# Performance work log

Measured on AMD Instinct MI355X. Metric: run time of the kernel, lower is better.

The kernel has to match this reference:

```python
import jax, jax.numpy as jnp
import numpy as np

N_NODES = 50000


def _relgraphconv(x, W, Wloop, b, src, dst, etypes, n_nodes):
    # DGL RelGraphConv (regularizer=None, self_loop=True, norm=None):
    # out[i] = sum over incoming edges (j->i, rel r) of W_r @ x[j]  +  W_loop @ x[i]  +  b
    # low-mem form: transform all nodes per relation, then gather per edge.
    h_rel = jnp.einsum('ni,rio->rno', x, W)          # [R, N, out]
    msg = h_rel[etypes, src]                          # [E, out]
    agg = jax.ops.segment_sum(msg, dst, num_segments=n_nodes)  # [N, out]
    return agg + x @ Wloop + b


def setup_inputs() -> dict:
    key = jax.random.key(0)
    ks = jax.random.split(key, 12)
    N, E, n_state = N_NODES, 800000, 128
    inp = {
        'x': jax.random.normal(ks[0], (N, n_state), dtype=jnp.float32),
        'src': jax.random.randint(ks[1], (E,), 0, N, dtype=jnp.int32),
        'dst': jax.random.randint(ks[2], (E,), 0, N, dtype=jnp.int32),
        'etypes': jax.random.randint(ks[3], (E,), 0, 2, dtype=jnp.int32),
        'cell_size': jax.random.randint(ks[4], (N,), 0, 8, dtype=jnp.int32),
        'max_size': jax.random.randint(ks[5], (N,), 0, 8, dtype=jnp.int32),
        'W1': jax.random.normal(ks[6], (2, n_state, 64), dtype=jnp.float32) * 0.05,
        'loop1': jax.random.normal(ks[7], (n_state, 64), dtype=jnp.float32) * 0.05,
        'b1': jnp.zeros((64,), dtype=jnp.float32),
        'W2': jax.random.normal(ks[8], (2, 64, 64), dtype=jnp.float32) * 0.05,
        'loop2': jax.random.normal(ks[9], (64, 64), dtype=jnp.float32) * 0.05,
        'b2': jnp.zeros((64,), dtype=jnp.float32),
        'W3': jax.random.normal(ks[10], (2, 64, 2), dtype=jnp.float32) * 0.05,
        'loop3': jax.random.normal(ks[11], (64, 2), dtype=jnp.float32) * 0.05,
        'b3': jnp.zeros((2,), dtype=jnp.float32),
    }
    return inp


def reference(x, src, dst, etypes, cell_size, max_size,
              W1, loop1, b1, W2, loop2, b2, W3, loop3, b3):
    N = x.shape[0]
    h = jax.nn.relu(_relgraphconv(x, W1, loop1, b1, src, dst, etypes, N))
    h = jax.nn.relu(_relgraphconv(h, W2, loop2, b2, src, dst, etypes, N))
    h = _relgraphconv(h, W3, loop3, b3, src, dst, etypes, N)   # [N, 2]
    # action mask: col 0 = cannot upsize, col 1 = cannot downsize
    upper = cell_size >= (max_size - 1)
    lower = cell_size == 0
    mask = jnp.stack([upper, lower], axis=1)                   # [N, 2] bool
    return jnp.where(mask, h.min() - 1.0, h)
```

## Files before the change

### kernel.cpp

```cpp
#include <hip/hip_runtime.h>


#define STRIDE 64
#define BINCAP 2560

typedef unsigned short ushortT;
typedef __attribute__((ext_vector_type(8))) short short8;
typedef __attribute__((ext_vector_type(4))) float f32x4;

__device__ inline ushortT f2bf(float f) {
    union { float f; unsigned u; } v; v.f = f;
    unsigned r = v.u + 0x7FFFu + ((v.u >> 16) & 1u);
    return (ushortT)(r >> 16);
}
__device__ inline float bf2f(ushortT h) {
    union { unsigned u; float f; } v; v.u = ((unsigned)h) << 16;
    return v.f;
}

__device__ inline void atomicMinF(float* addr, float v) {
    if (v >= 0.f) atomicMin((int*)addr, __float_as_int(v));
    else          atomicMax((unsigned int*)addr, __float_as_uint(v));
}

__global__ __launch_bounds__(256) void pack_init_kernel(
    const float* __restrict__ W1, const float* __restrict__ loop1,
    const float* __restrict__ W2, const float* __restrict__ loop2,
    ushortT* __restrict__ BP1, ushortT* __restrict__ BP2,
    int* __restrict__ bincnt, float* __restrict__ minval,
    int* __restrict__ done, int NBINS) {
    int g = (int)blockIdx.x * 256 + (int)threadIdx.x;
    if (g < NBINS) bincnt[g] = 0;
    if (g == 0) { *(int*)minval = 0x7f7f7f7f; *done = 0; }
    if (g < 3072) {
        int l = g & 63, ks = (g >> 6) & 3, ct = g >> 8;
        int c = ct * 16 + (l & 15);
        int mat = c >> 6, cc = c & 63;
        int kbase = ks * 32 + (l >> 4) * 8;
        ushortT* dstp = BP1 + (size_t)g * 8;
#pragma unroll
        for (int j = 0; j < 8; ++j) {
            int k = kbase + j;
            float v = (mat < 2) ? W1[((size_t)mat * 128 + k) * 64 + cc]
                                : loop1[(size_t)k * 64 + cc];
            dstp[j] = f2bf(v);
        }
    } else {
        int s = g - 3072;
        int l = s & 63, ks = (s >> 6) & 1, ct = s >> 7;
        int c = ct * 16 + (l & 15);
        int mat = c >> 6, cc = c & 63;
        int kbase = ks * 32 + (l >> 4) * 8;
        ushortT* dstp = BP2 + (size_t)s * 8;
#pragma unroll
        for (int j = 0; j < 8; ++j) {
            int k = kbase + j;
            float v = (mat < 2) ? W2[((size_t)mat * 64 + k) * 64 + cc]
                                : loop2[(size_t)k * 64 + cc];
            dstp[j] = f2bf(v);
        }
    }
}

__global__ __launch_bounds__(256) void k1_kernel(
    const float* __restrict__ x, const ushortT* __restrict__ BP1,
    const float* __restrict__ b1,
    ushortT* __restrict__ hrelb, ushortT* __restrict__ H1b,
    const int* __restrict__ src, const int* __restrict__ dst,
    const int* __restrict__ et, int* __restrict__ bincnt, int2* __restrict__ binbuf,
    int N, int E, int NBINS, int NBA) {
    __shared__ int hist[512];
    __shared__ int gbase[512];
    __shared__ ushortT rnk[4096];

    const int t = (int)threadIdx.x;

    if ((int)blockIdx.x < NBA) {
        for (int i = t; i < NBINS; i += 256) hist[i] = 0;
        __syncthreads();
        const int base = (int)blockIdx.x * 4096;
#pragma unroll
        for (int i = 0; i < 16; ++i) {
            int e = base + t + i * 256;
            if (e < E) {
                int bb = dst[e] >> 7;
                rnk[t + i * 256] = (ushortT)atomicAdd(&hist[bb], 1);
            }
        }
        __syncthreads();
        for (int i = t; i < NBINS; i += 256) {
            int h = hist[i];
            gbase[i] = h ? atomicAdd(&bincnt[i], h) : 0;
        }
        __syncthreads();
#pragma unroll
        for (int i = 0; i < 16; ++i) {
            int e = base + t + i * 256;
            if (e < E) {
                int dd = dst[e];
                int bb = dd >> 7;
                int v = et[e] * N + src[e];
                int pos = gbase[bb] + (int)rnk[t + i * 256];
                if (pos < BINCAP)
                    binbuf[(size_t)bb * BINCAP + pos] = make_int2(dd, v);
            }
        }
        return;
    }
    const int w = t >> 6, lane = t & 63;
    const int rowbase = (((int)blockIdx.x - NBA) * 4 + w) * 16;
    const int m = lane & 15, quad = lane >> 4;
    const int nclamp = min(rowbase + m, N - 1);

    short8 a[4];
    const float* xp = x + (size_t)nclamp * 128 + quad * 8;
#pragma unroll
    for (int ks = 0; ks < 4; ++ks) {
        float4 g0 = *(const float4*)(xp + ks * 32);
        float4 g1 = *(const float4*)(xp + ks * 32 + 4);
        a[ks][0] = (short)f2bf(g0.x); a[ks][1] = (short)f2bf(g0.y);
        a[ks][2] = (short)f2bf(g0.z); a[ks][3] = (short)f2bf(g0.w);
        a[ks][4] = (short)f2bf(g1.x); a[ks][5] = (short)f2bf(g1.y);
        a[ks][6] = (short)f2bf(g1.z); a[ks][7] = (short)f2bf(g1.w);
    }

    f32x4 acc[12];
#pragma unroll
    for (int ct = 0; ct < 12; ++ct) acc[ct] = (f32x4){0.f, 0.f, 0.f, 0.f};

#pragma unroll
    for (int ks = 0; ks < 4; ++ks) {
#pragma unroll
        for (int ct = 0; ct < 12; ++ct) {
            short8 b = *(const short8*)&BP1[((size_t)(ct * 4 + ks) * 64 + lane) * 8];
            acc[ct] = __builtin_amdgcn_mfma_f32_16x16x32_bf16(a[ks], b, acc[ct], 0, 0, 0);
        }
    }

    const int node0 = rowbase + quad * 4;
#pragma unroll
    for (int ct = 0; ct < 12; ++ct) {
        int c = ct * 16 + m;
        int mat = c >> 6, cc = c & 63;
        float bias = (mat == 2) ? b1[cc] : 0.f;
#pragma unroll
        for (int j = 0; j < 4; ++j) {
            int n = node0 + j;
            if (n < N) {
                float v = acc[ct][j] + bias;
                if (mat < 2) hrelb[((size_t)mat * N + n) * 64 + cc] = f2bf(v);
                else         H1b[(size_t)n * 64 + cc] = f2bf(v);
            }
        }
    }
}

__global__ __launch_bounds__(512, 4) void ag2_kernel(
    const ushortT* __restrict__ hrelb, const ushortT* __restrict__ H1b,
    const ushortT* __restrict__ BP2, const float* __restrict__ b2,
    const int* __restrict__ bincnt, const int2* __restrict__ binbuf,
    int* __restrict__ eidx, int* __restrict__ cnt,
    ushortT* __restrict__ hrel2b, ushortT* __restrict__ H2b, int N) {
    __shared__ int lcnt[64];
    __shared__ int lidx[64][STRIDE];
    __shared__ __align__(16) ushortT Hs[64][72];

    const int t = (int)threadIdx.x;
    const int B = (int)blockIdx.x;
    const int nodeBase = B * 64;
    const int bin = B >> 1;

    if (t < 64) lcnt[t] = 0;
    __syncthreads();

    const int cb = min(bincnt[bin], BINCAP);
    const int2* buf = binbuf + (size_t)bin * BINCAP;
    for (int i = t; i < cb; i += 512) {
        int2 rec = buf[i];
        int local = rec.x - nodeBase;
        if ((unsigned)local < 64u) {
            int r = atomicAdd(&lcnt[local], 1);
            if (r < STRIDE) {
                lidx[local][r] = rec.y;
                eidx[(size_t)rec.x * STRIDE + r] = rec.y;
            }
        }
    }
    __syncthreads();
    if (t < 64) {
        int c = min(lcnt[t], STRIDE);
        lcnt[t] = c;
        int node = nodeBase + t;
        if (node < N) cnt[node] = c;
    }
    __syncthreads();

    const int w = t >> 6, lane = t & 63;

    for (int i = 0; i < 8; ++i) {
        int local = w * 8 + i;
        int node = nodeBase + local;
        if (node >= N) { Hs[local][lane] = 0; continue; }
        int deg = lcnt[local];
        float acc = bf2f(H1b[(size_t)node * 64 + lane]);
        int j = 0;
        for (; j + 7 < deg; j += 8) {
            float v[8];
#pragma unroll
            for (int q = 0; q < 8; ++q) {
                int id = lidx[local][j + q];
                v[q] = bf2f(hrelb[(size_t)id * 64 + lane]);
            }
            acc += ((v[0] + v[1]) + (v[2] + v[3])) + ((v[4] + v[5]) + (v[6] + v[7]));
        }
        for (; j < deg; ++j)
            acc += bf2f(hrelb[(size_t)lidx[local][j] * 64 + lane]);
        Hs[local][lane] = f2bf(fmaxf(acc, 0.f));
    }
    __syncthreads();

    const int rt = w & 3, h = w >> 2;
    const int m = lane & 15, quad = lane >> 4;
    short8 a[2];
#pragma unroll
    for (int ks = 0; ks < 2; ++ks)
        a[ks] = *(const short8*)&Hs[rt * 16 + m][quad * 8 + ks * 32];

    f32x4 acc[6];
#pragma unroll
    for (int c6 = 0; c6 < 6; ++c6) acc[c6] = (f32x4){0.f, 0.f, 0.f, 0.f};

#pragma unroll
    for (int ks = 0; ks < 2; ++ks) {
#pragma unroll
        for (int c6 = 0; c6 < 6; ++c6) {
            int ct = h * 6 + c6;
            short8 b = *(const short8*)&BP2[((size_t)(ct * 2 + ks) * 64 + lane) * 8];
            acc[c6] = __builtin_amdgcn_mfma_f32_16x16x32_bf16(a[ks], b, acc[c6], 0, 0, 0);
        }
    }

    const int node0 = nodeBase + rt * 16 + quad * 4;
#pragma unroll
    for (int c6 = 0; c6 < 6; ++c6) {
        int ct = h * 6 + c6;
        int c = ct * 16 + m;
        int mat = c >> 6, cc = c & 63;
        float bias = (mat == 2) ? b2[cc] : 0.f;
#pragma unroll
        for (int j = 0; j < 4; ++j) {
            int n = node0 + j;
            if (n < N) {
                float v = acc[c6][j] + bias;
                if (mat < 2) hrel2b[((size_t)mat * N + n) * 64 + cc] = f2bf(v);
                else         H2b[(size_t)n * 64 + cc] = f2bf(v);
            }
        }
    }
}

__global__ void k3_kernel(const ushortT* __restrict__ hrel2b, const ushortT* __restrict__ H2b,
                          const int* __restrict__ eidx, const int* __restrict__ cnt,
                          const float* __restrict__ W3, const float* __restrict__ loop3,
                          const float* __restrict__ b3,
                          float* __restrict__ hrel3, float* __restrict__ H3, int N) {
    int node = (int)blockIdx.x * 4 + ((int)threadIdx.x >> 6);
    if (node >= N) return;
    int lane = (int)threadIdx.x & 63;
    int deg = cnt[node];
    int my = (lane < deg) ? eidx[(size_t)node * STRIDE + lane] : 0;
    float acc = bf2f(H2b[(size_t)node * 64 + lane]);
    int j = 0;
    for (; j + 7 < deg; j += 8) {
        int id[8];
        float v[8];
#pragma unroll
        for (int q = 0; q < 8; ++q) id[q] = __shfl(my, j + q, 64);
#pragma unroll
        for (int q = 0; q < 8; ++q) v[q] = bf2f(hrel2b[(size_t)id[q] * 64 + lane]);
        acc += ((v[0] + v[1]) + (v[2] + v[3])) + ((v[4] + v[5]) + (v[6] + v[7]));
    }
    for (; j < deg; ++j)
        acc += bf2f(hrel2b[(size_t)__shfl(my, j, 64) * 64 + lane]);
    float xk = fmaxf(acc, 0.f);
    float p[6];
    p[0] = xk * W3[lane * 2 + 0];
    p[1] = xk * W3[lane * 2 + 1];
    p[2] = xk * W3[(64 + lane) * 2 + 0];
    p[3] = xk * W3[(64 + lane) * 2 + 1];
    p[4] = xk * loop3[lane * 2 + 0];
    p[5] = xk * loop3[lane * 2 + 1];
#pragma unroll
    for (int mm = 32; mm >= 1; mm >>= 1) {
#pragma unroll
        for (int q = 0; q < 6; ++q) p[q] += __shfl_xor(p[q], mm, 64);
    }
    if (lane == 0) {
        hrel3[(size_t)node * 2 + 0] = p[0];
        hrel3[(size_t)node * 2 + 1] = p[1];
        hrel3[((size_t)N + node) * 2 + 0] = p[2];
        hrel3[((size_t)N + node) * 2 + 1] = p[3];
        H3[(size_t)node * 2 + 0] = p[4] + b3[0];
        H3[(size_t)node * 2 + 1] = p[5] + b3[1];
    }
}

__global__ __launch_bounds__(256) void a3m_mask_kernel(
    const float* __restrict__ hrel3, const int* __restrict__ eidx,
    const int* __restrict__ cnt, const float* __restrict__ H3,
    const int* __restrict__ cs, const int* __restrict__ ms,
    float* __restrict__ minval, int* __restrict__ done,
    float* __restrict__ out, int N) {
    const int t = (int)threadIdx.x;
    const int n = (int)blockIdx.x * 256 + t;
    float a0 = 0.f, a1 = 0.f;
    float v = 3.4e38f;
    if (n < N) {
        a0 = H3[n * 2 + 0]; a1 = H3[n * 2 + 1];
        int deg = cnt[n];
        const int* row = &eidx[(size_t)n * STRIDE];
        int j = 0;
        for (; j + 3 < deg; j += 4) {
            int i0 = row[j], i1 = row[j + 1], i2 = row[j + 2], i3 = row[j + 3];
            float2 q0 = *(const float2*)&hrel3[(size_t)i0 * 2];
            float2 q1 = *(const float2*)&hrel3[(size_t)i1 * 2];
            float2 q2 = *(const float2*)&hrel3[(size_t)i2 * 2];
            float2 q3 = *(const float2*)&hrel3[(size_t)i3 * 2];
            a0 += (q0.x + q1.x) + (q2.x + q3.x);
            a1 += (q0.y + q1.y) + (q2.y + q3.y);
        }
        for (; j < deg; ++j) {
            float2 q = *(const float2*)&hrel3[(size_t)row[j] * 2];
            a0 += q.x; a1 += q.y;
        }
        v = fminf(a0, a1);
    }
#pragma unroll
    for (int mm = 32; mm >= 1; mm >>= 1) v = fminf(v, __shfl_xor(v, mm, 64));
    __shared__ float s[4];
    __shared__ float gm;
    if ((t & 63) == 0) s[t >> 6] = v;
    __syncthreads();
    if (t == 0) {
        atomicMinF(minval, fminf(fminf(s[0], s[1]), fminf(s[2], s[3])));
        __threadfence();
        atomicAdd(done, 1);
        while (atomicAdd(done, 0) < (int)gridDim.x)
            __builtin_amdgcn_s_sleep(2);
        gm = atomicAdd(minval, 0.0f);
    }
    __syncthreads();
    if (n < N) {
        float mn = gm - 1.0f;
        bool up = cs[n] >= ms[n] - 1;
        bool lo = cs[n] == 0;
        out[n * 2 + 0] = up ? mn : a0;
        out[n * 2 + 1] = lo ? mn : a1;
    }
}

extern "C" void kernel_launch(void* const* d_in, const int* in_sizes, int n_in,
                              void* d_out, int out_size, void* d_ws, size_t ws_size,
                              hipStream_t stream) {
    const float* x     = (const float*)d_in[0];
    const int* src     = (const int*)d_in[1];
    const int* dst     = (const int*)d_in[2];
    const int* etypes  = (const int*)d_in[3];
    const int* cellsz  = (const int*)d_in[4];
    const int* maxsz   = (const int*)d_in[5];
    const float* W1    = (const float*)d_in[6];
    const float* loop1 = (const float*)d_in[7];
    const float* b1    = (const float*)d_in[8];
    const float* W2    = (const float*)d_in[9];
    const float* loop2 = (const float*)d_in[10];
    const float* b2    = (const float*)d_in[11];
    const float* W3    = (const float*)d_in[12];
    const float* loop3 = (const float*)d_in[13];
    const float* b3    = (const float*)d_in[14];
    float* out = (float*)d_out;

    const int N = in_sizes[0] / 128;
    const int E = in_sizes[1];

    char* p = (char*)d_ws;
    auto alloc = [&](size_t bytes) -> void* {
        void* r = (void*)p;
        p += ((bytes + 255) / 256) * 256;
        return r;
    };
    ushortT* hrelb  = (ushortT*)alloc((size_t)2 * N * 64 * 2);
    ushortT* H1b    = (ushortT*)alloc((size_t)N * 64 * 2);
    ushortT* hrel2b = (ushortT*)alloc((size_t)2 * N * 64 * 2);
    ushortT* H2b    = (ushortT*)alloc((size_t)N * 64 * 2);
    float* hrel3    = (float*)alloc((size_t)2 * N * 2 * 4);
    float* H3       = (float*)alloc((size_t)N * 2 * 4);
    int* cnt        = (int*)alloc((size_t)N * 4);
    int* eidx       = (int*)alloc((size_t)N * STRIDE * 4);
    ushortT* BP1    = (ushortT*)alloc((size_t)3072 * 8 * 2);
    ushortT* BP2    = (ushortT*)alloc((size_t)1536 * 8 * 2);
    float* minval   = (float*)alloc(4);
    int* done       = (int*)alloc(4);

    const int NBINS = (N + 127) >> 7;
    int* bincnt     = (int*)alloc((size_t)NBINS * 4);
    int2* binbuf    = (int2*)alloc((size_t)NBINS * BINCAP * 8);
    (void)ws_size; (void)n_in; (void)out_size;

    const int NB_N   = (N + 255) / 256;
    const int NTILES = (N + 63) / 64;
    const int NB_W   = (N + 3) / 4;
    const int NBA    = (E + 4095) / 4096;
    const int NB_AG  = (N + 63) / 64;

    pack_init_kernel<<<18, 256, 0, stream>>>(
        W1, loop1, W2, loop2, BP1, BP2, bincnt, minval, done, NBINS);

    k1_kernel<<<NBA + NTILES, 256, 0, stream>>>(
        x, BP1, b1, hrelb, H1b,
        src, dst, etypes, bincnt, binbuf, N, E, NBINS, NBA);

    ag2_kernel<<<NB_AG, 512, 0, stream>>>(
        hrelb, H1b, BP2, b2, bincnt, binbuf, eidx, cnt, hrel2b, H2b, N);

    k3_kernel<<<NB_W, 256, 0, stream>>>(hrel2b, H2b, eidx, cnt, W3, loop3, b3,
                                        hrel3, H3, N);

    a3m_mask_kernel<<<NB_N, 256, 0, stream>>>(hrel3, eidx, cnt, H3,
                                              cellsz, maxsz, minval, done, out, N);
}
```

Measured before the change: 219.1 us.

## Fuse all graph-conv stages into one persistent kernel with grid barriers

Replaces the four separate stage kernels with one persistent kernel of 512 blocks. Blocks pull work units from atomic work queues for the binning/GEMM1 stage and the aggregation/GEMM2 stage, and use a grid-stride loop for layer 3. The stages are separated by spin-wait global barriers, which removes the kernel launch gaps and tail effects between stages. The trade-offs are fixed grid sizing, spin-barrier overhead, and a dependence on every block being resident at once to avoid deadlock.

```diff
diff --git a/kernel.cpp b/kernel.cpp
--- a/kernel.cpp
+++ b/kernel.cpp
@@ -21,6 +21,17 @@
 __device__ inline void atomicMinF(float* addr, float v) {
     if (v >= 0.f) atomicMin((int*)addr, __float_as_int(v));
     else          atomicMax((unsigned int*)addr, __float_as_uint(v));
+}
+
+__device__ inline void gbar(int* bar, int target) {
+    __syncthreads();
+    if (threadIdx.x == 0) {
+        __threadfence();
+        atomicAdd(bar, 1);
+        while (atomicAdd(bar, 0) < target) __builtin_amdgcn_s_sleep(8);
+        __threadfence();
+    }
+    __syncthreads();
 }
 
 __global__ __launch_bounds__(256) void pack_init_kernel(
@@ -28,10 +39,10 @@
     const float* __restrict__ W2, const float* __restrict__ loop2,
     ushortT* __restrict__ BP1, ushortT* __restrict__ BP2,
     int* __restrict__ bincnt, float* __restrict__ minval,
-    int* __restrict__ done, int NBINS) {
+    int* __restrict__ bar, int* __restrict__ wq, int NBINS) {
     int g = (int)blockIdx.x * 256 + (int)threadIdx.x;
     if (g < NBINS) bincnt[g] = 0;
-    if (g == 0) { *(int*)minval = 0x7f7f7f7f; *done = 0; }
+    if (g == 0) { *(int*)minval = 0x7f7f7f7f; bar[0] = 0; wq[0] = 0; wq[1] = 0; }
     if (g < 3072) {
         int l = g & 63, ks = (g >> 6) & 3, ct = g >> 8;
         int c = ct * 16 + (l & 15);
@@ -62,257 +73,258 @@
     }
 }
 
-__global__ __launch_bounds__(256) void k1_kernel(
+__global__ __launch_bounds__(512, 4) void mega_kernel(
     const float* __restrict__ x, const ushortT* __restrict__ BP1,
-    const float* __restrict__ b1,
+    const ushortT* __restrict__ BP2,
+    const float* __restrict__ b1, const float* __restrict__ b2,
+    const int* __restrict__ src, const int* __restrict__ dst,
+    const int* __restrict__ et,
+    int* __restrict__ bincnt, int2* __restrict__ binbuf,
     ushortT* __restrict__ hrelb, ushortT* __restrict__ H1b,
-    const int* __restrict__ src, const int* __restrict__ dst,
-    const int* __restrict__ et, int* __restrict__ bincnt, int2* __restrict__ binbuf,
-    int N, int E, int NBINS, int NBA) {
-    __shared__ int hist[512];
-    __shared__ int gbase[512];
-    __shared__ ushortT rnk[4096];
+    ushortT* __restrict__ hrel2b, ushortT* __restrict__ H2b,
+    int* __restrict__ eidx, int* __restrict__ cnt,
+    const float* __restrict__ W3, const float* __restrict__ loop3,
+    const float* __restrict__ b3,
+    float* __restrict__ hrel3, float* __restrict__ H3,
+    const int* __restrict__ cs, const int* __restrict__ ms,
+    float* __restrict__ minval, int* __restrict__ bar, int* __restrict__ wq,
+    float* __restrict__ out,
+    int N, int E, int NBINS, int NBA, int NU1, int NU2) {
+    __shared__ __align__(16) char smemraw[25856];
+    __shared__ int uS;
+    __shared__ float gmS;
 
     const int t = (int)threadIdx.x;
-
-    if ((int)blockIdx.x < NBA) {
-        for (int i = t; i < NBINS; i += 256) hist[i] = 0;
-        __syncthreads();
-        const int base = (int)blockIdx.x * 4096;
-#pragma unroll
-        for (int i = 0; i < 16; ++i) {
-            int e = base + t + i * 256;
-            if (e < E) {
-                int bb = dst[e] >> 7;
-                rnk[t + i * 256] = (ushortT)atomicAdd(&hist[bb], 1);
+    const int w = t >> 6, lane = t & 63;
+    const int NB = (int)gridDim.x;
+
+    {
+        int* hist = (int*)smemraw;
+        int* gb   = hist + 512;
+        ushortT* rnk = (ushortT*)(gb + 512);
+        for (;;) {
+            if (t == 0) uS = atomicAdd(&wq[0], 1);
+            __syncthreads();
+            const int u = uS;
+            __syncthreads();
+            if (u >= NU1) break;
+            if (u < NBA) {
+                for (int i = t; i < NBINS; i += 512) hist[i] = 0;
+                __syncthreads();
+                const int base = u * 4096;
+#pragma unroll
+                for (int i = 0; i < 8; ++i) {
+                    int e = base + t + i * 512;
+                    if (e < E) {
+                        int bb = dst[e] >> 7;
+                        rnk[t + i * 512] = (ushortT)atomicAdd(&hist[bb], 1);
+                    }
+                }
+                __syncthreads();
+                for (int i = t; i < NBINS; i += 512) {
+                    int h = hist[i];
+                    gb[i] = h ? atomicAdd(&bincnt[i], h) : 0;
+                }
+                __syncthreads();
+#pragma unroll
+                for (int i = 0; i < 8; ++i) {
+                    int e = base + t + i * 512;
+                    if (e < E) {
+                        int dd = dst[e];
+                        int bb = dd >> 7;
+                        int v = et[e] * N + src[e];
+                        int pos = gb[bb] + (int)rnk[t + i * 512];
+                        if (pos < BINCAP)
+                            binbuf[(size_t)bb * BINCAP + pos] = make_int2(dd, v);
+                    }
+                }
+            } else {
+                const int u2 = u - NBA;
+                const int rowbase = (u2 * 8 + w) * 16;
+                const int m = lane & 15, quad = lane >> 4;
+                const int nclamp = min(rowbase + m, N - 1);
+
+                short8 a[4];
+                const float* xp = x + (size_t)nclamp * 128 + quad * 8;
+#pragma unroll
+                for (int ks = 0; ks < 4; ++ks) {
+                    float4 g0 = *(const float4*)(xp + ks * 32);
+                    float4 g1 = *(const float4*)(xp + ks * 32 + 4);
+                    a[ks][0] = (short)f2bf(g0.x); a[ks][1] = (short)f2bf(g0.y);
+                    a[ks][2] = (short)f2bf(g0.z); a[ks][3] = (short)f2bf(g0.w);
+                    a[ks][4] = (short)f2bf(g1.x); a[ks][5] = (short)f2bf(g1.y);
+                    a[ks][6] = (short)f2bf(g1.z); a[ks][7] = (short)f2bf(g1.w);
+                }
+                f32x4 acc[12];
+#pragma unroll
+                for (int ct = 0; ct < 12; ++ct) acc[ct] = (f32x4){0.f, 0.f, 0.f, 0.f};
+#pragma unroll
+                for (int ks = 0; ks < 4; ++ks) {
+#pragma unroll
+                    for (int ct = 0; ct < 12; ++ct) {
+                        short8 b = *(const short8*)&BP1[((size_t)(ct * 4 + ks) * 64 + lane) * 8];
+                        acc[ct] = __builtin_amdgcn_mfma_f32_16x16x32_bf16(a[ks], b, acc[ct], 0, 0, 0);
+                    }
+                }
+                const int node0 = rowbase + quad * 4;
+#pragma unroll
+                for (int ct = 0; ct < 12; ++ct) {
+                    int c = ct * 16 + m;
+                    int mat = c >> 6, cc = c & 63;
+                    float bias = (mat == 2) ? b1[cc] : 0.f;
+#pragma unroll
+                    for (int j = 0; j < 4; ++j) {
+                        int n = node0 + j;
+                        if (n < N) {
+                            float v = acc[ct][j] + bias;
+                            if (mat < 2) hrelb[((size_t)mat * N + n) * 64 + cc] = f2bf(v);
+                            else         H1b[(size_t)n * 64 + cc] = f2bf(v);
+                        }
+                    }
+                }
             }
         }
-        __syncthreads();
-        for (int i = t; i < NBINS; i += 256) {
-            int h = hist[i];
-            gbase[i] = h ? atomicAdd(&bincnt[i], h) : 0;
-        }
-        __syncthreads();
-#pragma unroll
-        for (int i = 0; i < 16; ++i) {
-            int e = base + t + i * 256;
-            if (e < E) {
-                int dd = dst[e];
-                int bb = dd >> 7;
-                int v = et[e] * N + src[e];
-                int pos = gbase[bb] + (int)rnk[t + i * 256];
-                if (pos < BINCAP)
-                    binbuf[(size_t)bb * BINCAP + pos] = make_int2(dd, v);
+    }
+    gbar(bar, NB);
+
+    {
+        int* lcnt = (int*)smemraw;
+        int* lidx = lcnt + 64;
+        ushortT* Hs = (ushortT*)(lidx + 64 * STRIDE);
+        for (;;) {
+            if (t == 0) uS = atomicAdd(&wq[1], 1);
+            __syncthreads();
+            const int u = uS;
+            __syncthreads();
+            if (u >= NU2) break;
+            const int nodeBase = u * 64;
+            const int bin = u >> 1;
+            if (t < 64) lcnt[t] = 0;
+            __syncthreads();
+            const int cb = min(bincnt[bin], BINCAP);
+            const int2* buf = binbuf + (size_t)bin * BINCAP;
+            for (int i = t; i < cb; i += 512) {
+                int2 rec = buf[i];
+                int local = rec.x - nodeBase;
+                if ((unsigned)local < 64u) {
+                    int r = atomicAdd(&lcnt[local], 1);
+                    if (r < STRIDE) {
+                        lidx[local * STRIDE + r] = rec.y;
+                        eidx[(size_t)rec.x * STRIDE + r] = rec.y;
+                    }
+                }
             }
-        }
-        return;
-    }
-    const int w = t >> 6, lane = t & 63;
-    const int rowbase = (((int)blockIdx.x - NBA) * 4 + w) * 16;
-    const int m = lane & 15, quad = lane >> 4;
-    const int nclamp = min(rowbase + m, N - 1);
-
-    short8 a[4];
-    const float* xp = x + (size_t)nclamp * 128 + quad * 8;
-#pragma unroll
-    for (int ks = 0; ks < 4; ++ks) {
-        float4 g0 = *(const float4*)(xp + ks * 32);
-        float4 g1 = *(const float4*)(xp + ks * 32 + 4);
-        a[ks][0] = (short)f2bf(g0.x); a[ks][1] = (short)f2bf(g0.y);
-        a[ks][2] = (short)f2bf(g0.z); a[ks][3] = (short)f2bf(g0.w);
-        a[ks][4] = (short)f2bf(g1.x); a[ks][5] = (short)f2bf(g1.y);
-        a[ks][6] = (short)f2bf(g1.z); a[ks][7] = (short)f2bf(g1.w);
-    }
-
-    f32x4 acc[12];
-#pragma unroll
-    for (int ct = 0; ct < 12; ++ct) acc[ct] = (f32x4){0.f, 0.f, 0.f, 0.f};
-
-#pragma unroll
-    for (int ks = 0; ks < 4; ++ks) {
-#pragma unroll
-        for (int ct = 0; ct < 12; ++ct) {
-            short8 b = *(const short8*)&BP1[((size_t)(ct * 4 + ks) * 64 + lane) * 8];
-            acc[ct] = __builtin_amdgcn_mfma_f32_16x16x32_bf16(a[ks], b, acc[ct], 0, 0, 0);
-        }
-    }
-
-    const int node0 = rowbase + quad * 4;
-#pragma unroll
-    for (int ct = 0; ct < 12; ++ct) {
-        int c = ct * 16 + m;
-        int mat = c >> 6, cc = c & 63;
-        float bias = (mat == 2) ? b1[cc] : 0.f;
-#pragma unroll
-        for (int j = 0; j < 4; ++j) {
-            int n = node0 + j;
-            if (n < N) {
-                float v = acc[ct][j] + bias;
-                if (mat < 2) hrelb[((size_t)mat * N + n) * 64 + cc] = f2bf(v);
-                else         H1b[(size_t)n * 64 + cc] = f2bf(v);
+            __syncthreads();
+            if (t < 64) {
+                int c = min(lcnt[t], STRIDE);
+                lcnt[t] = c;
+                int node = nodeBase + t;
+                if (node < N) cnt[node] = c;
             }
-        }
-    }
-}
-
-__global__ __launch_bounds__(512, 4) void ag2_kernel(
-    const ushortT* __restrict__ hrelb, const ushortT* __restrict__ H1b,
-    const ushortT* __restrict__ BP2, const float* __restrict__ b2,
-    const int* __restrict__ bincnt, const int2* __restrict__ binbuf,
-    int* __restrict__ eidx, int* __restrict__ cnt,
-    ushortT* __restrict__ hrel2b, ushortT* __restrict__ H2b, int N) {
-    __shared__ int lcnt[64];
-    __shared__ int lidx[64][STRIDE];
-    __shared__ __align__(16) ushortT Hs[64][72];
-
-    const int t = (int)threadIdx.x;
-    const int B = (int)blockIdx.x;
-    const int nodeBase = B * 64;
-    const int bin = B >> 1;
-
-    if (t < 64) lcnt[t] = 0;
-    __syncthreads();
-
-    const int cb = min(bincnt[bin], BINCAP);
-    const int2* buf = binbuf + (size_t)bin * BINCAP;
-    for (int i = t; i < cb; i += 512) {
-        int2 rec = buf[i];
-        int local = rec.x - nodeBase;
-        if ((unsigned)local < 64u) {
-            int r = atomicAdd(&lcnt[local], 1);
-            if (r < STRIDE) {
-                lidx[local][r] = rec.y;
-                eidx[(size_t)rec.x * STRIDE + r] = rec.y;
+            __syncthreads();
+            for (int i = 0; i < 8; ++i) {
+                int local = w * 8 + i;
+                int node = nodeBase + local;
+                if (node >= N) { Hs[local * 72 + lane] = 0; continue; }
+                int deg = lcnt[local];
+                float acc = bf2f(H1b[(size_t)node * 64 + lane]);
+                int j = 0;
+                for (; j + 7 < deg; j += 8) {
+                    float v[8];
+#pragma unroll
+                    for (int q = 0; q < 8; ++q) {
+                        int id = lidx[local * STRIDE + j + q];
+                        v[q] = bf2f(hrelb[(size_t)id * 64 + lane]);
+                    }
+                    acc += ((v[0] + v[1]) + (v[2] + v[3])) + ((v[4] + v[5]) + (v[6] + v[7]));
+                }
+                for (; j < deg; ++j)
+                    acc += bf2f(hrelb[(size_t)lidx[local * STRIDE + j] * 64 + lane]);
+                Hs[local * 72 + lane] = f2bf(fmaxf(acc, 0.f));
             }
-        }
-    }
-    __syncthreads();
-    if (t < 64) {
-        int c = min(lcnt[t], STRIDE);
-        lcnt[t] = c;
-        int node = nodeBase + t;
-        if (node < N) cnt[node] = c;
-    }
-    __syncthreads();
-
-    const int w = t >> 6, lane = t & 63;
-
-    for (int i = 0; i < 8; ++i) {
-        int local = w * 8 + i;
-        int node = nodeBase + local;
-        if (node >= N) { Hs[local][lane] = 0; continue; }
-        int deg = lcnt[local];
-        float acc = bf2f(H1b[(size_t)node * 64 + lane]);
+            __syncthreads();
+            {
+                const int rt = w & 3, h = w >> 2;
+                const int m = lane & 15, quad = lane >> 4;
+                short8 a[2];
+#pragma unroll
+                for (int ks = 0; ks < 2; ++ks)
+                    a[ks] = *(const short8*)&Hs[(rt * 16 + m) * 72 + quad * 8 + ks * 32];
+                f32x4 acc[6];
+#pragma unroll
+                for (int c6 = 0; c6 < 6; ++c6) acc[c6] = (f32x4){0.f, 0.f, 0.f, 0.f};
+#pragma unroll
+                for (int ks = 0; ks < 2; ++ks) {
+#pragma unroll
+                    for (int c6 = 0; c6 < 6; ++c6) {
+                        int ct = h * 6 + c6;
+                        short8 b = *(const short8*)&BP2[((size_t)(ct * 2 + ks) * 64 + lane) * 8];
+                        acc[c6] = __builtin_amdgcn_mfma_f32_16x16x32_bf16(a[ks], b, acc[c6], 0, 0, 0);
+                    }
+                }
+                const int node0 = nodeBase + rt * 16 + quad * 4;
+#pragma unroll
+                for (int c6 = 0; c6 < 6; ++c6) {
+                    int ct = h * 6 + c6;
+                    int c = ct * 16 + m;
+                    int mat = c >> 6, cc = c & 63;
+                    float bias = (mat == 2) ? b2[cc] : 0.f;
+#pragma unroll
+                    for (int j = 0; j < 4; ++j) {
+                        int n = node0 + j;
+                        if (n < N) {
+                            float v = acc[c6][j] + bias;
+                            if (mat < 2) hrel2b[((size_t)mat * N + n) * 64 + cc] = f2bf(v);
+                            else         H2b[(size_t)n * 64 + cc] = f2bf(v);
+                        }
+                    }
+                }
+            }
+        }
+    }
+    gbar(bar, NB * 2);
+
+    for (int node = (int)blockIdx.x * 8 + w; node < N; node += NB * 8) {
+        int deg = cnt[node];
+        int my = (lane < deg) ? eidx[(size_t)node * STRIDE + lane] : 0;
+        float acc = bf2f(H2b[(size_t)node * 64 + lane]);
         int j = 0;
         for (; j + 7 < deg; j += 8) {
+            int id[8];
             float v[8];
 #pragma unroll
-            for (int q = 0; q < 8; ++q) {
-                int id = lidx[local][j + q];
-                v[q] = bf2f(hrelb[(size_t)id * 64 + lane]);
-            }
+            for (int q = 0; q < 8; ++q) id[q] = __shfl(my, j + q, 64);
+#pragma unroll
+            for (int q = 0; q < 8; ++q) v[q] = bf2f(hrel2b[(size_t)id[q] * 64 + lane]);
             acc += ((v[0] + v[1]) + (v[2] + v[3])) + ((v[4] + v[5]) + (v[6] + v[7]));
         }
         for (; j < deg; ++j)
-            acc += bf2f(hrelb[(size_t)lidx[local][j] * 64 + lane]);
-        Hs[local][lane] = f2bf(fmaxf(acc, 0.f));
-    }
-    __syncthreads();
-
-    const int rt = w & 3, h = w >> 2;
-    const int m = lane & 15, quad = lane >> 4;
-    short8 a[2];
-#pragma unroll
-    for (int ks = 0; ks < 2; ++ks)
-        a[ks] = *(const short8*)&Hs[rt * 16 + m][quad * 8 + ks * 32];
-
-    f32x4 acc[6];
-#pragma unroll
-    for (int c6 = 0; c6 < 6; ++c6) acc[c6] = (f32x4){0.f, 0.f, 0.f, 0.f};
-
-#pragma unroll
-    for (int ks = 0; ks < 2; ++ks) {
-#pragma unroll
-        for (int c6 = 0; c6 < 6; ++c6) {
-            int ct = h * 6 + c6;
-            short8 b = *(const short8*)&BP2[((size_t)(ct * 2 + ks) * 64 + lane) * 8];
-            acc[c6] = __builtin_amdgcn_mfma_f32_16x16x32_bf16(a[ks], b, acc[c6], 0, 0, 0);
-        }
-    }
-
-    const int node0 = nodeBase + rt * 16 + quad * 4;
-#pragma unroll
-    for (int c6 = 0; c6 < 6; ++c6) {
-        int ct = h * 6 + c6;
-        int c = ct * 16 + m;
-        int mat = c >> 6, cc = c & 63;
-        float bias = (mat == 2) ? b2[cc] : 0.f;
-#pragma unroll
-        for (int j = 0; j < 4; ++j) {
-            int n = node0 + j;
-            if (n < N) {
-                float v = acc[c6][j] + bias;
-                if (mat < 2) hrel2b[((size_t)mat * N + n) * 64 + cc] = f2bf(v);
-                else         H2b[(size_t)n * 64 + cc] = f2bf(v);
-            }
-        }
-    }
-}
-
-__global__ void k3_kernel(const ushortT* __restrict__ hrel2b, const ushortT* __restrict__ H2b,
-                          const int* __restrict__ eidx, const int* __restrict__ cnt,
-                          const float* __restrict__ W3, const float* __restrict__ loop3,
-                          const float* __restrict__ b3,
-                          float* __restrict__ hrel3, float* __restrict__ H3, int N) {
-    int node = (int)blockIdx.x * 4 + ((int)threadIdx.x >> 6);
-    if (node >= N) return;
-    int lane = (int)threadIdx.x & 63;
-    int deg = cnt[node];
-    int my = (lane < deg) ? eidx[(size_t)node * STRIDE + lane] : 0;
-    float acc = bf2f(H2b[(size_t)node * 64 + lane]);
-    int j = 0;
-    for (; j + 7 < deg; j += 8) {
-        int id[8];
-        float v[8];
-#pragma unroll
-        for (int q = 0; q < 8; ++q) id[q] = __shfl(my, j + q, 64);
-#pragma unroll
-        for (int q = 0; q < 8; ++q) v[q] = bf2f(hrel2b[(size_t)id[q] * 64 + lane]);
-        acc += ((v[0] + v[1]) + (v[2] + v[3])) + ((v[4] + v[5]) + (v[6] + v[7]));
-    }
-    for (; j < deg; ++j)
-        acc += bf2f(hrel2b[(size_t)__shfl(my, j, 64) * 64 + lane]);
-    float xk = fmaxf(acc, 0.f);
-    float p[6];
-    p[0] = xk * W3[lane * 2 + 0];
-    p[1] = xk * W3[lane * 2 + 1];
-    p[2] = xk * W3[(64 + lane) * 2 + 0];
-    p[3] = xk * W3[(64 + lane) * 2 + 1];
-    p[4] = xk * loop3[lane * 2 + 0];
-    p[5] = xk * loop3[lane * 2 + 1];
-#pragma unroll
-    for (int mm = 32; mm >= 1; mm >>= 1) {
-#pragma unroll
-        for (int q = 0; q < 6; ++q) p[q] += __shfl_xor(p[q], mm, 64);
-    }
-    if (lane == 0) {
-        hrel3[(size_t)node * 2 + 0] = p[0];
-        hrel3[(size_t)node * 2 + 1] = p[1];
-        hrel3[((size_t)N + node) * 2 + 0] = p[2];
-        hrel3[((size_t)N + node) * 2 + 1] = p[3];
-        H3[(size_t)node * 2 + 0] = p[4] + b3[0];
-        H3[(size_t)node * 2 + 1] = p[5] + b3[1];
-    }
-}
-
-__global__ __launch_bounds__(256) void a3m_mask_kernel(
-    const float* __restrict__ hrel3, const int* __restrict__ eidx,
-    const int* __restrict__ cnt, const float* __restrict__ H3,
-    const int* __restrict__ cs, const int* __restrict__ ms,
-    float* __restrict__ minval, int* __restrict__ done,
-    float* __restrict__ out, int N) {
-    const int t = (int)threadIdx.x;
-    const int n = (int)blockIdx.x * 256 + t;
+            acc += bf2f(hrel2b[(size_t)__shfl(my, j, 64) * 64 + lane]);
+        float xk = fmaxf(acc, 0.f);
+        float p[6];
+        p[0] = xk * W3[lane * 2 + 0];
+        p[1] = xk * W3[lane * 2 + 1];
+        p[2] = xk * W3[(64 + lane) * 2 + 0];
+        p[3] = xk * W3[(64 + lane) * 2 + 1];
+        p[4] = xk * loop3[lane * 2 + 0];
+        p[5] = xk * loop3[lane * 2 + 1];
+#pragma unroll
+        for (int mm = 32; mm >= 1; mm >>= 1) {
+#pragma unroll
+            for (int q = 0; q < 6; ++q) p[q] += __shfl_xor(p[q], mm, 64);
+        }
+        if (lane == 0) {
+            hrel3[(size_t)node * 2 + 0] = p[0];
+            hrel3[(size_t)node * 2 + 1] = p[1];
+            hrel3[((size_t)N + node) * 2 + 0] = p[2];
+            hrel3[((size_t)N + node) * 2 + 1] = p[3];
+            H3[(size_t)node * 2 + 0] = p[4] + b3[0];
+            H3[(size_t)node * 2 + 1] = p[5] + b3[1];
+        }
+    }
+    gbar(bar, NB * 3);
+
+    const int n = (int)blockIdx.x * 512 + t;
     float a0 = 0.f, a1 = 0.f;
     float v = 3.4e38f;
     if (n < N) {
@@ -337,21 +349,23 @@
     }
 #pragma unroll
     for (int mm = 32; mm >= 1; mm >>= 1) v = fminf(v, __shfl_xor(v, mm, 64));
-    __shared__ float s[4];
-    __shared__ float gm;
-    if ((t & 63) == 0) s[t >> 6] = v;
-    __syncthreads();
-    if (t == 0) {
-        atomicMinF(minval, fminf(fminf(s[0], s[1]), fminf(s[2], s[3])));
-        __threadfence();
-        atomicAdd(done, 1);
-        while (atomicAdd(done, 0) < (int)gridDim.x)
-            __builtin_amdgcn_s_sleep(2);
-        gm = atomicAdd(minval, 0.0f);
-    }
+    {
+        float* s = (float*)smemraw;
+        __syncthreads();
+        if (lane == 0) s[w] = v;
+        __syncthreads();
+        if (t == 0) {
+            float bm = s[0];
+#pragma unroll
+            for (int k = 1; k < 8; ++k) bm = fminf(bm, s[k]);
+            atomicMinF(minval, bm);
+        }
+    }
+    gbar(bar, NB * 4);
+    if (t == 0) gmS = atomicAdd(minval, 0.0f);
     __syncthreads();
     if (n < N) {
-        float mn = gm - 1.0f;
+        float mn = gmS - 1.0f;
         bool up = cs[n] >= ms[n] - 1;
         bool lo = cs[n] == 0;
         out[n * 2 + 0] = up ? mn : a0;
@@ -399,32 +413,26 @@
     ushortT* BP1    = (ushortT*)alloc((size_t)3072 * 8 * 2);
     ushortT* BP2    = (ushortT*)alloc((size_t)1536 * 8 * 2);
     float* minval   = (float*)alloc(4);
-    int* done       = (int*)alloc(4);
+    int* bar        = (int*)alloc(4);
+    int* wq         = (int*)alloc(8);
 
     const int NBINS = (N + 127) >> 7;
     int* bincnt     = (int*)alloc((size_t)NBINS * 4);
     int2* binbuf    = (int2*)alloc((size_t)NBINS * BINCAP * 8);
     (void)ws_size; (void)n_in; (void)out_size;
 
-    const int NB_N   = (N + 255) / 256;
-    const int NTILES = (N + 63) / 64;
-    const int NB_W   = (N + 3) / 4;
-    const int NBA    = (E + 4095) / 4096;
-    const int NB_AG  = (N + 63) / 64;
+    const int NBA = (E + 4095) / 4096;
+    const int NT1 = (N + 127) / 128;
+    const int NU1 = NBA + NT1;
+    const int NU2 = (N + 63) / 64;
 
     pack_init_kernel<<<18, 256, 0, stream>>>(
-        W1, loop1, W2, loop2, BP1, BP2, bincnt, minval, done, NBINS);
-
-    k1_kernel<<<NBA + NTILES, 256, 0, stream>>>(
-        x, BP1, b1, hrelb, H1b,
-        src, dst, etypes, bincnt, binbuf, N, E, NBINS, NBA);
-
-    ag2_kernel<<<NB_AG, 512, 0, stream>>>(
-        hrelb, H1b, BP2, b2, bincnt, binbuf, eidx, cnt, hrel2b, H2b, N);
-
-    k3_kernel<<<NB_W, 256, 0, stream>>>(hrel2b, H2b, eidx, cnt, W3, loop3, b3,
-                                        hrel3, H3, N);
-
-    a3m_mask_kernel<<<NB_N, 256, 0, stream>>>(hrel3, eidx, cnt, H3,
-                                              cellsz, maxsz, minval, done, out, N);
-}
+        W1, loop1, W2, loop2, BP1, BP2, bincnt, minval, bar, wq, NBINS);
+
+    mega_kernel<<<512, 512, 0, stream>>>(
+        x, BP1, BP2, b1, b2, src, dst, etypes, bincnt, binbuf,
+        hrelb, H1b, hrel2b, H2b, eidx, cnt,
+        W3, loop3, b3, hrel3, H3, cellsz, maxsz,
+        minval, bar, wq, out,
+        N, E, NBINS, NBA, NU1, NU2);
+}
```

Measured after the change: 493.3 us. +125.1%, slower.

## Fuse layer-3 transform and final aggregate/mask into one persistent kernel

Applied to the files above, without the earlier changes.

Merges the layer-3 per-node transform kernel and the final aggregation/min/mask kernel into a single persistent kernel. It launches 2048 blocks that loop over nodes, then separates the two phases with a hierarchical grid barrier built from per-group and global counters. This removes a kernel launch and the boundary between the two kernels. It relies on all 2048 blocks being resident at once; if they are not, the barrier can deadlock. Separately, the layer-2 aggregation now broadcasts neighbor indices with readlane from a register instead of reading them repeatedly from shared memory.

```diff
diff --git a/kernel.cpp b/kernel.cpp
--- a/kernel.cpp
+++ b/kernel.cpp
@@ -3,6 +3,7 @@
 
 #define STRIDE 64
 #define BINCAP 2560
+#define TAILNB 2048
 
 typedef unsigned short ushortT;
 typedef __attribute__((ext_vector_type(8))) short short8;
@@ -21,6 +22,21 @@
 __device__ inline void atomicMinF(float* addr, float v) {
     if (v >= 0.f) atomicMin((int*)addr, __float_as_int(v));
     else          atomicMax((unsigned int*)addr, __float_as_uint(v));
+}
+
+__device__ inline void gbar2(int* ctr, int b) {
+    __syncthreads();
+    if (threadIdx.x == 0) {
+        __threadfence();
+        const int g = (int)blockIdx.x >> 8;
+        int* grp  = ctr + (size_t)(b * 9 + g) * 64;
+        int* glob = ctr + (size_t)(b * 9 + 8) * 64;
+        if (atomicAdd(grp, 1) == 255) atomicAdd(glob, 1);
+        while (__hip_atomic_load(glob, __ATOMIC_RELAXED, __HIP_MEMORY_SCOPE_AGENT) < 8)
+            __builtin_amdgcn_s_sleep(4);
+        __threadfence();
+    }
+    __syncthreads();
 }
 
 __global__ __launch_bounds__(256) void pack_init_kernel(
@@ -28,10 +44,11 @@
     const float* __restrict__ W2, const float* __restrict__ loop2,
     ushortT* __restrict__ BP1, ushortT* __restrict__ BP2,
     int* __restrict__ bincnt, float* __restrict__ minval,
-    int* __restrict__ done, int NBINS) {
+    int* __restrict__ barctr, int NBINS) {
     int g = (int)blockIdx.x * 256 + (int)threadIdx.x;
     if (g < NBINS) bincnt[g] = 0;
-    if (g == 0) { *(int*)minval = 0x7f7f7f7f; *done = 0; }
+    if (g < 1152) barctr[g] = 0;
+    if (g == 0) *(int*)minval = 0x7f7f7f7f;
     if (g < 3072) {
         int l = g & 63, ks = (g >> 6) & 3, ct = g >> 8;
         int c = ct * 16 + (l & 15);
@@ -202,19 +219,22 @@
         int node = nodeBase + local;
         if (node >= N) { Hs[local][lane] = 0; continue; }
         int deg = lcnt[local];
+        int my = lidx[local][lane];
         float acc = bf2f(H1b[(size_t)node * 64 + lane]);
         int j = 0;
         for (; j + 7 < deg; j += 8) {
             float v[8];
 #pragma unroll
             for (int q = 0; q < 8; ++q) {
-                int id = lidx[local][j + q];
+                int id = __builtin_amdgcn_readlane(my, j + q);
                 v[q] = bf2f(hrelb[(size_t)id * 64 + lane]);
             }
             acc += ((v[0] + v[1]) + (v[2] + v[3])) + ((v[4] + v[5]) + (v[6] + v[7]));
         }
-        for (; j < deg; ++j)
-            acc += bf2f(hrelb[(size_t)lidx[local][j] * 64 + lane]);
+        for (; j < deg; ++j) {
+            int id = __builtin_amdgcn_readlane(my, j);
+            acc += bf2f(hrelb[(size_t)id * 64 + lane]);
+        }
         Hs[local][lane] = f2bf(fmaxf(acc, 0.f));
     }
     __syncthreads();
@@ -259,59 +279,62 @@
     }
 }
 
-__global__ void k3_kernel(const ushortT* __restrict__ hrel2b, const ushortT* __restrict__ H2b,
-                          const int* __restrict__ eidx, const int* __restrict__ cnt,
-                          const float* __restrict__ W3, const float* __restrict__ loop3,
-                          const float* __restrict__ b3,
-                          float* __restrict__ hrel3, float* __restrict__ H3, int N) {
-    int node = (int)blockIdx.x * 4 + ((int)threadIdx.x >> 6);
-    if (node >= N) return;
-    int lane = (int)threadIdx.x & 63;
-    int deg = cnt[node];
-    int my = (lane < deg) ? eidx[(size_t)node * STRIDE + lane] : 0;
-    float acc = bf2f(H2b[(size_t)node * 64 + lane]);
-    int j = 0;
-    for (; j + 7 < deg; j += 8) {
-        int id[8];
-        float v[8];
-#pragma unroll
-        for (int q = 0; q < 8; ++q) id[q] = __shfl(my, j + q, 64);
-#pragma unroll
-        for (int q = 0; q < 8; ++q) v[q] = bf2f(hrel2b[(size_t)id[q] * 64 + lane]);
-        acc += ((v[0] + v[1]) + (v[2] + v[3])) + ((v[4] + v[5]) + (v[6] + v[7]));
-    }
-    for (; j < deg; ++j)
-        acc += bf2f(hrel2b[(size_t)__shfl(my, j, 64) * 64 + lane]);
-    float xk = fmaxf(acc, 0.f);
-    float p[6];
-    p[0] = xk * W3[lane * 2 + 0];
-    p[1] = xk * W3[lane * 2 + 1];
-    p[2] = xk * W3[(64 + lane) * 2 + 0];
-    p[3] = xk * W3[(64 + lane) * 2 + 1];
-    p[4] = xk * loop3[lane * 2 + 0];
-    p[5] = xk * loop3[lane * 2 + 1];
-#pragma unroll
-    for (int mm = 32; mm >= 1; mm >>= 1) {
-#pragma unroll
-        for (int q = 0; q < 6; ++q) p[q] += __shfl_xor(p[q], mm, 64);
-    }
-    if (lane == 0) {
-        hrel3[(size_t)node * 2 + 0] = p[0];
-        hrel3[(size_t)node * 2 + 1] = p[1];
-        hrel3[((size_t)N + node) * 2 + 0] = p[2];
-        hrel3[((size_t)N + node) * 2 + 1] = p[3];
-        H3[(size_t)node * 2 + 0] = p[4] + b3[0];
-        H3[(size_t)node * 2 + 1] = p[5] + b3[1];
-    }
-}
-
-__global__ __launch_bounds__(256) void a3m_mask_kernel(
-    const float* __restrict__ hrel3, const int* __restrict__ eidx,
-    const int* __restrict__ cnt, const float* __restrict__ H3,
+__global__ __launch_bounds__(256, 8) void tail_kernel(
+    const ushortT* __restrict__ hrel2b, const ushortT* __restrict__ H2b,
+    const int* __restrict__ eidx, const int* __restrict__ cnt,
+    const float* __restrict__ W3, const float* __restrict__ loop3,
+    const float* __restrict__ b3,
     const int* __restrict__ cs, const int* __restrict__ ms,
-    float* __restrict__ minval, int* __restrict__ done,
+    float* __restrict__ hrel3, float* __restrict__ H3,
+    float* __restrict__ minval, int* __restrict__ barctr,
     float* __restrict__ out, int N) {
     const int t = (int)threadIdx.x;
+    const int w = t >> 6, lane = t & 63;
+
+    const float w3a = W3[lane * 2 + 0], w3b = W3[lane * 2 + 1];
+    const float w3c = W3[(64 + lane) * 2 + 0], w3d = W3[(64 + lane) * 2 + 1];
+    const float l3a = loop3[lane * 2 + 0], l3b = loop3[lane * 2 + 1];
+    for (int node = (int)blockIdx.x * 4 + w; node < N; node += TAILNB * 4) {
+        int deg = cnt[node];
+        int my = eidx[(size_t)node * STRIDE + lane];
+        float acc = bf2f(H2b[(size_t)node * 64 + lane]);
+        int j = 0;
+        for (; j + 7 < deg; j += 8) {
+            float v[8];
+#pragma unroll
+            for (int q = 0; q < 8; ++q) {
+                int id = __builtin_amdgcn_readlane(my, j + q);
+                v[q] = bf2f(hrel2b[(size_t)id * 64 + lane]);
+            }
+            acc += ((v[0] + v[1]) + (v[2] + v[3])) + ((v[4] + v[5]) + (v[6] + v[7]));
+        }
+        for (; j < deg; ++j) {
+            int id = __builtin_amdgcn_readlane(my, j);
+            acc += bf2f(hrel2b[(size_t)id * 64 + lane]);
+        }
+        float xk = fmaxf(acc, 0.f);
+        float p0 = xk * w3a, p1 = xk * w3b, p2 = xk * w3c;
+        float p3 = xk * w3d, p4 = xk * l3a, p5 = xk * l3b;
+#pragma unroll
+        for (int mm = 32; mm >= 1; mm >>= 1) {
+            p0 += __shfl_xor(p0, mm, 64);
+            p1 += __shfl_xor(p1, mm, 64);
+            p2 += __shfl_xor(p2, mm, 64);
+            p3 += __shfl_xor(p3, mm, 64);
+            p4 += __shfl_xor(p4, mm, 64);
+            p5 += __shfl_xor(p5, mm, 64);
+        }
+        if (lane == 0) {
+            hrel3[(size_t)node * 2 + 0] = p0;
+            hrel3[(size_t)node * 2 + 1] = p1;
+            hrel3[((size_t)N + node) * 2 + 0] = p2;
+            hrel3[((size_t)N + node) * 2 + 1] = p3;
+            H3[(size_t)node * 2 + 0] = p4 + b3[0];
+            H3[(size_t)node * 2 + 1] = p5 + b3[1];
+        }
+    }
+    gbar2(barctr, 0);
+
     const int n = (int)blockIdx.x * 256 + t;
     float a0 = 0.f, a1 = 0.f;
     float v = 3.4e38f;
@@ -337,21 +360,20 @@
     }
 #pragma unroll
     for (int mm = 32; mm >= 1; mm >>= 1) v = fminf(v, __shfl_xor(v, mm, 64));
-    __shared__ float s[4];
-    __shared__ float gm;
-    if ((t & 63) == 0) s[t >> 6] = v;
-    __syncthreads();
-    if (t == 0) {
-        atomicMinF(minval, fminf(fminf(s[0], s[1]), fminf(s[2], s[3])));
-        __threadfence();
-        atomicAdd(done, 1);
-        while (atomicAdd(done, 0) < (int)gridDim.x)
-            __builtin_amdgcn_s_sleep(2);
-        gm = atomicAdd(minval, 0.0f);
-    }
+    {
+        __shared__ float s[4];
+        if (lane == 0) s[w] = v;
+        __syncthreads();
+        if (t == 0)
+            atomicMinF(minval, fminf(fminf(s[0], s[1]), fminf(s[2], s[3])));
+    }
+    gbar2(barctr, 1);
+
+    __shared__ float gmS;
+    if (t == 0) gmS = atomicAdd(minval, 0.0f);
     __syncthreads();
     if (n < N) {
-        float mn = gm - 1.0f;
+        float mn = gmS - 1.0f;
         bool up = cs[n] >= ms[n] - 1;
         bool lo = cs[n] == 0;
         out[n * 2 + 0] = up ? mn : a0;
@@ -399,21 +421,19 @@
     ushortT* BP1    = (ushortT*)alloc((size_t)3072 * 8 * 2);
     ushortT* BP2    = (ushortT*)alloc((size_t)1536 * 8 * 2);
     float* minval   = (float*)alloc(4);
-    int* done       = (int*)alloc(4);
+    int* barctr     = (int*)alloc((size_t)1152 * 4);
 
     const int NBINS = (N + 127) >> 7;
     int* bincnt     = (int*)alloc((size_t)NBINS * 4);
     int2* binbuf    = (int2*)alloc((size_t)NBINS * BINCAP * 8);
     (void)ws_size; (void)n_in; (void)out_size;
 
-    const int NB_N   = (N + 255) / 256;
+    const int NBA    = (E + 4095) / 4096;
     const int NTILES = (N + 63) / 64;
-    const int NB_W   = (N + 3) / 4;
-    const int NBA    = (E + 4095) / 4096;
     const int NB_AG  = (N + 63) / 64;
 
     pack_init_kernel<<<18, 256, 0, stream>>>(
-        W1, loop1, W2, loop2, BP1, BP2, bincnt, minval, done, NBINS);
+        W1, loop1, W2, loop2, BP1, BP2, bincnt, minval, barctr, NBINS);
 
     k1_kernel<<<NBA + NTILES, 256, 0, stream>>>(
         x, BP1, b1, hrelb, H1b,
@@ -422,9 +442,7 @@
     ag2_kernel<<<NB_AG, 512, 0, stream>>>(
         hrelb, H1b, BP2, b2, bincnt, binbuf, eidx, cnt, hrel2b, H2b, N);
 
-    k3_kernel<<<NB_W, 256, 0, stream>>>(hrel2b, H2b, eidx, cnt, W3, loop3, b3,
-                                        hrel3, H3, N);
-
-    a3m_mask_kernel<<<NB_N, 256, 0, stream>>>(hrel3, eidx, cnt, H3,
-                                              cellsz, maxsz, minval, done, out, N);
-}
+    tail_kernel<<<TAILNB, 256, 0, stream>>>(
+        hrel2b, H2b, eidx, cnt, W3, loop3, b3, cellsz, maxsz,
+        hrel3, H3, minval, barctr, out, N);
+}
```

Measured after the change: 360.7 us. 64.6% more time.
